# Kernel optimization log

Measured on AMD Instinct MI355X. Metric: run time of the kernel, lower is better.

Reference implementation:

```python
import jax, jax.numpy as jnp
import numpy as np

GROUPS = 8
EPS = 1e-5


def setup_inputs() -> dict:
    key = jax.random.key(0)
    ks = jax.random.split(key, 7)
    b, c, h, w = 32, 256, 32, 32
    x = jax.random.normal(ks[0], (b, c, h, w), dtype=jnp.float32)
    gn_weight = jax.random.normal(ks[1], (c,), dtype=jnp.float32) * 0.02 + 1.0
    gn_bias = jax.random.normal(ks[2], (c,), dtype=jnp.float32) * 0.02
    w_qkv = jax.random.normal(ks[3], (3 * c, c), dtype=jnp.float32) / np.sqrt(c)
    b_qkv = jax.random.normal(ks[4], (3 * c,), dtype=jnp.float32) * 0.01
    w_out = jax.random.normal(ks[5], (c, c), dtype=jnp.float32) / np.sqrt(c)
    b_out = jax.random.normal(ks[6], (c,), dtype=jnp.float32) * 0.01
    return {"x": x, "gn_weight": gn_weight, "gn_bias": gn_bias,
            "w_qkv": w_qkv, "b_qkv": b_qkv, "w_out": w_out, "b_out": b_out}


def group_norm(x, weight, bias):
    b, c, h, w = x.shape
    xg = x.reshape(b, GROUPS, c // GROUPS, h, w)
    mean = jnp.mean(xg, axis=(2, 3, 4), keepdims=True)
    var = jnp.var(xg, axis=(2, 3, 4), keepdims=True)
    xg = (xg - mean) * jax.lax.rsqrt(var + EPS)
    x = xg.reshape(b, c, h, w)
    return x * weight[None, :, None, None] + bias[None, :, None, None]


def reference(x, gn_weight, gn_bias, w_qkv, b_qkv, w_out, b_out):
    b, c, h, w = x.shape
    x_norm = group_norm(x, gn_weight, gn_bias)
    # 1x1 conv == channel matmul: (b, 3c, h, w)
    qkv = jnp.einsum('oc,bchw->bohw', w_qkv, x_norm) + b_qkv[None, :, None, None]
    q, k, v = jnp.split(qkv, 3, axis=1)
    hw = h * w
    q = q.reshape(b, c, hw)  # used transposed: (b, hw, c)
    k = k.reshape(b, c, hw)
    v = v.reshape(b, c, hw)
    scale = 1.0 / jnp.sqrt(jnp.float32(c))
    attn = jax.nn.softmax(jnp.einsum('bcs,bct->bst', q, k) * scale, axis=-1)  # (b, hw, hw)
    out = jnp.einsum('bst,bct->bcs', attn, v).reshape(b, c, h, w)
    out = jnp.einsum('oc,bchw->bohw', w_out, out) + b_out[None, :, None, None]
    return out + x
```

## Files before the change

### kernel.cpp

```cpp
#include <hip/hip_runtime.h>
#include <hip/hip_bf16.h>


typedef __bf16 bf16x8 __attribute__((ext_vector_type(8)));
typedef __bf16 bf16x4 __attribute__((ext_vector_type(4)));
typedef float f32x4 __attribute__((ext_vector_type(4)));
typedef float f32x16 __attribute__((ext_vector_type(16)));

#define MFMA16(a, b, c) __builtin_amdgcn_mfma_f32_16x16x32_bf16(a, b, c, 0, 0, 0)
#define MFMA32(a, b, c) __builtin_amdgcn_mfma_f32_32x32x16_bf16(a, b, c, 0, 0, 0)

#define GLD16(gsrc_, ldst_)                                                                  \
    __builtin_amdgcn_global_load_lds((const __attribute__((address_space(1))) void*)(gsrc_), \
                                     (__attribute__((address_space(3))) void*)(ldst_), 16, 0, 0)

__global__ __launch_bounds__(256) void gn_stats(const float* __restrict__ x,
                                                float* __restrict__ stats,
                                                const float* __restrict__ wqkv,
                                                const float* __restrict__ wout,
                                                __bf16* __restrict__ wbf) {
    const int bid = blockIdx.x, t = threadIdx.x;
    if (bid < 128) {
        int idx = (bid * 256 + t) * 8;
        const float* src = (idx < 196608) ? (wqkv + idx) : (wout + (idx - 196608));
        float4 v0 = *(const float4*)src;
        float4 v1 = *(const float4*)(src + 4);
        bf16x8 o;
        o[0] = (__bf16)v0.x; o[1] = (__bf16)v0.y; o[2] = (__bf16)v0.z; o[3] = (__bf16)v0.w;
        o[4] = (__bf16)v1.x; o[5] = (__bf16)v1.y; o[6] = (__bf16)v1.z; o[7] = (__bf16)v1.w;
        *(bf16x8*)&wbf[idx] = o;
    }
    const int bg = bid >> 3, part = bid & 7;
    const float* xp = x + (size_t)bg * 32768 + part * 4096;
    float s = 0.f, s2 = 0.f;
    #pragma unroll
    for (int i = 0; i < 4; i++) {
        float4 v = *(const float4*)(xp + (i * 256 + t) * 4);
        s  += v.x + v.y + v.z + v.w;
        s2 += v.x*v.x + v.y*v.y + v.z*v.z + v.w*v.w;
    }
    #pragma unroll
    for (int o = 32; o > 0; o >>= 1) { s += __shfl_down(s, o, 64); s2 += __shfl_down(s2, o, 64); }
    __shared__ float red[8];
    const int wv = t >> 6;
    if ((t & 63) == 0) { red[wv * 2] = s; red[wv * 2 + 1] = s2; }
    __syncthreads();
    if (t == 0) {
        float ts  = red[0] + red[2] + red[4] + red[6];
        float ts2 = red[1] + red[3] + red[5] + red[7];
        stats[bg * 16 + part * 2]     = ts;
        stats[bg * 16 + part * 2 + 1] = ts2;
    }
}

__global__ __launch_bounds__(512) void gn_apply(const float* __restrict__ x,
                                                const float* __restrict__ stats,
                                                const float* __restrict__ gw,
                                                const float* __restrict__ gb,
                                                __bf16* __restrict__ xnT) {
    const int bid = blockIdx.x;
    const int bg = bid >> 3, part = bid & 7;
    const int b = bg >> 3, g = bg & 7;
    const int t = threadIdx.x;
    float ts = 0.f, ts2 = 0.f;
    #pragma unroll
    for (int p = 0; p < 8; p++) { ts += stats[bg * 16 + p * 2]; ts2 += stats[bg * 16 + p * 2 + 1]; }
    const float mean = ts / 32768.f;
    const float inv = rsqrtf(ts2 / 32768.f - mean * mean + 1e-5f);
    __shared__ __bf16 Lds[128][48];
    const int c = t >> 4, ss = (t & 15) * 8;
    const float ga = gw[g * 32 + c], be = gb[g * 32 + c];
    const float* xp = x + (((size_t)b * 256 + g * 32 + c) * 1024) + part * 128 + ss;
    float4 v0 = *(const float4*)xp;
    float4 v1 = *(const float4*)(xp + 4);
    float vv[8] = {v0.x, v0.y, v0.z, v0.w, v1.x, v1.y, v1.z, v1.w};
    #pragma unroll
    for (int i = 0; i < 8; i++) Lds[ss + i][c] = (__bf16)((vv[i] - mean) * inv * ga + be);
    __syncthreads();
    const int row = t >> 2, cb = (t & 3) * 8;
    bf16x8 ov = *(const bf16x8*)&Lds[row][cb];
    *(bf16x8*)&xnT[((size_t)b * 1024 + part * 128 + row) * 256 + g * 32 + cb] = ov;
}

#define GEMM64G_BODY(ArowBase_, BrowBase_)                                              \
    f32x4 acc[4][4] = {};                                                               \
    for (int kk = 0; kk < 256; kk += 64) {                                              \
        _Pragma("unroll")                                                               \
        for (int i = 0; i < 4; i++) {                                                   \
            const int ch = wave * 4 + i;                                                \
            const int r = ch * 8 + (lane >> 3);                                         \
            const int sw = ((lane & 7) ^ (r & 7)) * 8;                                  \
            GLD16((ArowBase_) + (size_t)r * 256 + kk + sw, (char*)&As[0][0] + ch * 1024); \
            GLD16((BrowBase_) + (size_t)r * 256 + kk + sw, (char*)&Bs[0][0] + ch * 1024); \
        }                                                                               \
        __syncthreads();                                                                \
        _Pragma("unroll")                                                               \
        for (int kh = 0; kh < 2; kh++) {                                                \
            bf16x8 af[4], bfv[4];                                                       \
            _Pragma("unroll")                                                           \
            for (int im = 0; im < 4; im++) {                                            \
                const int row = wm + im * 16 + l16;                                     \
                af[im] = *(const bf16x8*)&As[row][(((kh * 4 + quad) ^ (row & 7)) * 8)]; \
            }                                                                           \
            _Pragma("unroll")                                                           \
            for (int in = 0; in < 4; in++) {                                            \
                const int row = wn + in * 16 + l16;                                     \
                bfv[in] = *(const bf16x8*)&Bs[row][(((kh * 4 + quad) ^ (row & 7)) * 8)]; \
            }                                                                           \
            _Pragma("unroll")                                                           \
            for (int im = 0; im < 4; im++)                                              \
                _Pragma("unroll")                                                       \
                for (int in = 0; in < 4; in++)                                          \
                    acc[im][in] = MFMA16(af[im], bfv[in], acc[im][in]);                 \
        }                                                                               \
        __syncthreads();                                                                \
    }

__global__ __launch_bounds__(256) void qkv_gemm(const __bf16* __restrict__ wbf,
                                                const float* __restrict__ bias,
                                                const __bf16* __restrict__ xnT,
                                                __bf16* __restrict__ qtr,
                                                __bf16* __restrict__ ktr,
                                                __bf16* __restrict__ vbuf) {
    __shared__ union {
        struct { __bf16 A[128][64]; __bf16 B[128][64]; } g;
        __bf16 ct[128][136];
    } sm;
    const int lin = blockIdx.x + ((blockIdx.y + blockIdx.z * 6) << 3);
    const int xcd = lin & 7, idx = lin >> 3;
    const int gwk = xcd * 192 + idx;
    const int mt = gwk % 6, panel = gwk / 6;
    const int b = panel >> 3;
    const int n0 = (panel & 7) * 128, m0 = mt * 128;
    const int t = threadIdx.x;
    const int wave = t >> 6, lane = t & 63, quad = lane >> 4, l16 = lane & 15;
    const int wm = (wave & 1) * 64, wn = (wave >> 1) * 64;
    const __bf16* arow = wbf + (size_t)m0 * 256;
    const __bf16* brow = xnT + ((size_t)b * 1024 + n0) * 256;
    auto As = sm.g.A;
    auto Bs = sm.g.B;

    GEMM64G_BODY(arow, brow)

    if (m0 < 512) {
        #pragma unroll
        for (int im = 0; im < 4; im++) {
            #pragma unroll
            for (int in = 0; in < 4; in++) {
                int ob = m0 + wm + im * 16 + quad * 4;
                bf16x4 ov;
                #pragma unroll
                for (int r = 0; r < 4; r++) ov[r] = (__bf16)(acc[im][in][r] + bias[ob + r]);
                *(bf16x4*)&sm.ct[wn + in * 16 + l16][wm + im * 16 + quad * 4] = ov;
            }
        }
        __syncthreads();
        {
            const int rbase = t >> 2, cf = t & 3;
            #pragma unroll
            for (int rr = 0; rr < 2; rr++) {
                int row = rbase + rr * 64;
                int sg = n0 + row;
                __bf16* dst = (m0 < 256) ? &qtr[((size_t)b * 1024 + sg) * 256 + m0]
                                         : &ktr[((size_t)b * 1024 + sg) * 256 + (m0 - 256)];
                #pragma unroll
                for (int u = 0; u < 4; u++) {
                    int colb = cf * 8 + u * 32;
                    *(bf16x8*)&dst[colb] = *(const bf16x8*)&sm.ct[row][colb];
                }
            }
        }
    } else {
        #pragma unroll
        for (int im = 0; im < 4; im++) {
            #pragma unroll
            for (int in = 0; in < 4; in++) {
                int cl = wm + im * 16 + quad * 4;
                int tl = wn + in * 16 + l16;
                #pragma unroll
                for (int r = 0; r < 4; r++)
                    sm.ct[cl + r][tl] = (__bf16)(acc[im][in][r] + bias[m0 + cl + r]);
            }
        }
        __syncthreads();
        {
            const int row = t >> 1, tc = (t & 1) * 64;
            const int cglob = m0 - 512 + row;
            __bf16* dst = &vbuf[((size_t)b * 256 + cglob) * 1024 + n0 + tc];
            #pragma unroll
            for (int u = 0; u < 8; u++)
                *(bf16x8*)&dst[u * 8] = *(const bf16x8*)&sm.ct[row][tc + u * 8];
        }
    }
}

__global__ __launch_bounds__(512, 2) void attn_kernel(const __bf16* __restrict__ qtr,
                                                      const __bf16* __restrict__ ktr,
                                                      const __bf16* __restrict__ vbuf,
                                                      __bf16* __restrict__ aoT) {
    __shared__ __bf16 Kt[2][32][260];
    __shared__ __bf16 Vs[2][256][36];
    __shared__ bf16x8 Pl[4][2][2][64];
    __shared__ float Lred[4][2][32];
    const int b = blockIdx.x;
    const int tid = threadIdx.x;
    const int wave = tid >> 6, lane = tid & 63, half = lane >> 5, l31 = lane & 31;
    const int pair = wave & 3, th = wave >> 2;
    const int s0 = blockIdx.y * 128 + pair * 32;
    const float kscale = 0.09016844f;

    bf16x8 aq[16];
    #pragma unroll
    for (int ks = 0; ks < 16; ks++)
        aq[ks] = *(const bf16x8*)&qtr[((size_t)b * 1024 + s0 + l31) * 256 + ks * 16 + half * 8];

    const int k_row = tid >> 3;
    const int k_cb  = (tid & 7) * 8;
    const int v_c   = tid >> 1;
    const int v_th  = tid & 1;
    const size_t kbase = (size_t)b * 1024 * 256;
    const size_t vbase = (size_t)b * 256 * 1024;

    float l_acc = 0.f;
    f32x16 o_acc[4] = {};

    bf16x8 kpre[4], vpre[4];
    #pragma unroll
    for (int u = 0; u < 4; u++) {
        kpre[u] = *(const bf16x8*)&ktr[kbase + (size_t)k_row * 256 + k_cb + u * 64];
        vpre[u] = *(const bf16x8*)&vbuf[vbase + (size_t)v_c * 1024 + v_th * 32 + u * 8];
    }

    for (int it = 0; it < 16; it++) {
        #pragma unroll
        for (int u = 0; u < 4; u++)
            *(bf16x8*)&Kt[k_row >> 5][k_row & 31][k_cb + u * 64] = kpre[u];
        #pragma unroll
        for (int u = 0; u < 4; u++) {
            const bf16x4* hv = (const bf16x4*)&vpre[u];
            const int sbase = (u >> 1) * 16 + (u & 1) * 4;
            *(bf16x4*)&Vs[v_th][v_c][sbase]     = hv[0];
            *(bf16x4*)&Vs[v_th][v_c][sbase + 8] = hv[1];
        }
        __syncthreads();
        if (it < 15) {
            const int t1 = (it + 1) * 64;
            #pragma unroll
            for (int u = 0; u < 4; u++) {
                kpre[u] = *(const bf16x8*)&ktr[kbase + (size_t)(t1 + k_row) * 256 + k_cb + u * 64];
                vpre[u] = *(const bf16x8*)&vbuf[vbase + (size_t)v_c * 1024 + t1 + v_th * 32 + u * 8];
            }
        }

        f32x16 sc_a = {}, sc_b = {};
        __builtin_amdgcn_s_setprio(1);
        #pragma unroll
        for (int ks = 0; ks < 8; ks++) {
            bf16x8 bk0 = *(const bf16x8*)&Kt[th][l31][ks * 16 + half * 8];
            bf16x8 bk1 = *(const bf16x8*)&Kt[th][l31][(ks + 8) * 16 + half * 8];
            sc_a = MFMA32(bk0, aq[ks], sc_a);
            sc_b = MFMA32(bk1, aq[ks + 8], sc_b);
        }
        __builtin_amdgcn_s_setprio(0);

        bf16x8 pf0, pf1;
        #pragma unroll
        for (int r = 0; r < 8; r++) {
            float p = exp2f((sc_a[r] + sc_b[r]) * kscale);
            l_acc += p;
            pf0[r] = (__bf16)p;
        }
        #pragma unroll
        for (int r = 8; r < 16; r++) {
            float p = exp2f((sc_a[r] + sc_b[r]) * kscale);
            l_acc += p;
            pf1[r - 8] = (__bf16)p;
        }
        Pl[pair][th][0][lane] = pf0;
        Pl[pair][th][1][lane] = pf1;
        __syncthreads();
        bf16x8 pp0 = Pl[pair][1 - th][0][lane];
        bf16x8 pp1 = Pl[pair][1 - th][1][lane];

        bf16x8 ap[4];
        if (th == 0) { ap[0] = pf0; ap[1] = pf1; ap[2] = pp0; ap[3] = pp1; }
        else         { ap[0] = pp0; ap[1] = pp1; ap[2] = pf0; ap[3] = pf1; }

        __builtin_amdgcn_s_setprio(1);
        #pragma unroll
        for (int n = 0; n < 4; n++) {
            int c = th * 128 + n * 32 + l31;
            #pragma unroll
            for (int kc = 0; kc < 4; kc++) {
                bf16x8 bv = *(const bf16x8*)&Vs[kc >> 1][c][(kc & 1) * 16 + half * 8];
                o_acc[n] = MFMA32(ap[kc], bv, o_acc[n]);
            }
        }
        __builtin_amdgcn_s_setprio(0);
        __syncthreads();
    }

    l_acc += __shfl_xor(l_acc, 32, 64);
    if (lane < 32) Lred[pair][th][l31] = l_acc;
    __syncthreads();
    #pragma unroll
    for (int r = 0; r < 16; r++) {
        int row = (r & 3) + 8 * (r >> 2) + 4 * half;
        float rinv = 1.0f / (Lred[pair][0][row] + Lred[pair][1][row]);
        #pragma unroll
        for (int n = 0; n < 4; n++) {
            int c = th * 128 + n * 32 + l31;
            aoT[((size_t)b * 1024 + s0 + row) * 256 + c] = (__bf16)(o_acc[n][r] * rinv);
        }
    }
}

__global__ __launch_bounds__(256) void proj_gemm(const __bf16* __restrict__ wbf_out,
                                                 const float* __restrict__ bias,
                                                 const __bf16* __restrict__ aoT,
                                                 const float* __restrict__ resid,
                                                 float* __restrict__ Out) {
    __shared__ union {
        struct { __bf16 A[128][64]; __bf16 B[128][64]; } g;
        float cf[64][132];
    } sm;
    const int lin = blockIdx.x + ((blockIdx.y + blockIdx.z * 2) << 3);
    const int xcd = lin & 7, idx = lin >> 3;
    const int gwk = xcd * 64 + idx;
    const int mt = gwk & 1, panel = gwk >> 1;
    const int b = panel >> 3;
    const int n0 = (panel & 7) * 128, m0 = mt * 128;
    const int t = threadIdx.x;
    const int wave = t >> 6, lane = t & 63, quad = lane >> 4, l16 = lane & 15;
    const int wm = (wave & 1) * 64, wn = (wave >> 1) * 64;
    const __bf16* arow = wbf_out + (size_t)m0 * 256;
    const __bf16* brow = aoT + ((size_t)b * 1024 + n0) * 256;
    auto As = sm.g.A;
    auto Bs = sm.g.B;

    GEMM64G_BODY(arow, brow)

    for (int h = 0; h < 2; h++) {
        if ((wave & 1) == h) {
            #pragma unroll
            for (int im = 0; im < 4; im++)
                #pragma unroll
                for (int in = 0; in < 4; in++)
                    #pragma unroll
                    for (int r = 0; r < 4; r++)
                        sm.cf[im * 16 + quad * 4 + r][wn + in * 16 + l16] = acc[im][in][r];
        }
        __syncthreads();
        {
            const int rloc = t >> 2, cq = (t & 3) * 4;
            const int o = m0 + h * 64 + rloc;
            const float bo = bias[o];
            const float* rrow = &resid[((size_t)b * 256 + o) * 1024 + n0];
            float* orow = &Out[((size_t)b * 256 + o) * 1024 + n0];
            #pragma unroll
            for (int u = 0; u < 8; u++) {
                int col = cq + u * 16;
                f32x4 cv = *(const f32x4*)&sm.cf[rloc][col];
                float4 rv = *(const float4*)&rrow[col];
                float4 ov;
                ov.x = cv[0] + bo + rv.x;
                ov.y = cv[1] + bo + rv.y;
                ov.z = cv[2] + bo + rv.z;
                ov.w = cv[3] + bo + rv.w;
                *(float4*)&orow[col] = ov;
            }
        }
        __syncthreads();
    }
}

extern "C" void kernel_launch(void* const* d_in, const int* in_sizes, int n_in,
                              void* d_out, int out_size, void* d_ws, size_t ws_size,
                              hipStream_t stream) {
    const float* x    = (const float*)d_in[0];
    const float* gw   = (const float*)d_in[1];
    const float* gb   = (const float*)d_in[2];
    const float* wqkv = (const float*)d_in[3];
    const float* bqkv = (const float*)d_in[4];
    const float* wout = (const float*)d_in[5];
    const float* bout = (const float*)d_in[6];
    float* out = (float*)d_out;

    const size_t T16 = (size_t)32 * 1024 * 256;
    __bf16* xnT  = (__bf16*)d_ws;
    __bf16* qtr  = xnT + T16;
    __bf16* ktr  = qtr + T16;
    __bf16* vbuf = ktr + T16;
    __bf16* aoT  = vbuf + T16;
    __bf16* wbf  = aoT + T16;
    float* gstats = (float*)(wbf + 262144);

    gn_stats<<<dim3(2048), 256, 0, stream>>>(x, gstats, wqkv, wout, wbf);
    gn_apply<<<dim3(2048), 512, 0, stream>>>(x, gstats, gw, gb, xnT);
    qkv_gemm<<<dim3(8, 6, 32), 256, 0, stream>>>(wbf, bqkv, xnT, qtr, ktr, vbuf);
    attn_kernel<<<dim3(32, 8), 512, 0, stream>>>(qtr, ktr, vbuf, aoT);
    proj_gemm<<<dim3(8, 2, 32), 256, 0, stream>>>(wbf + 196608, bout, aoT, x, out);
}
```

Measured before the change: 186.4 us.

## Double-buffer LDS tiles in QKV and projection GEMMs; vectorize gn_apply LDS writes

Result: no change. 185.2 us (-0.6%).

```diff
diff --git a/kernel.cpp b/kernel.cpp
--- a/kernel.cpp
+++ b/kernel.cpp
@@ -67,45 +67,67 @@
     for (int p = 0; p < 8; p++) { ts += stats[bg * 16 + p * 2]; ts2 += stats[bg * 16 + p * 2 + 1]; }
     const float mean = ts / 32768.f;
     const float inv = rsqrtf(ts2 / 32768.f - mean * mean + 1e-5f);
-    __shared__ __bf16 Lds[128][48];
+    __shared__ __bf16 Lds[32][136];
     const int c = t >> 4, ss = (t & 15) * 8;
     const float ga = gw[g * 32 + c], be = gb[g * 32 + c];
     const float* xp = x + (((size_t)b * 256 + g * 32 + c) * 1024) + part * 128 + ss;
     float4 v0 = *(const float4*)xp;
     float4 v1 = *(const float4*)(xp + 4);
     float vv[8] = {v0.x, v0.y, v0.z, v0.w, v1.x, v1.y, v1.z, v1.w};
-    #pragma unroll
-    for (int i = 0; i < 8; i++) Lds[ss + i][c] = (__bf16)((vv[i] - mean) * inv * ga + be);
+    bf16x8 wv;
+    #pragma unroll
+    for (int i = 0; i < 8; i++) wv[i] = (__bf16)((vv[i] - mean) * inv * ga + be);
+    *(bf16x8*)&Lds[c][ss] = wv;
     __syncthreads();
     const int row = t >> 2, cb = (t & 3) * 8;
-    bf16x8 ov = *(const bf16x8*)&Lds[row][cb];
+    bf16x8 ov;
+    #pragma unroll
+    for (int j = 0; j < 8; j++) ov[j] = Lds[cb + j][row];
     *(bf16x8*)&xnT[((size_t)b * 1024 + part * 128 + row) * 256 + g * 32 + cb] = ov;
 }
 
-#define GEMM64G_BODY(ArowBase_, BrowBase_)                                              \
+#define GEMM64P_BODY(ArowBase_, BrowBase_)                                              \
     f32x4 acc[4][4] = {};                                                               \
-    for (int kk = 0; kk < 256; kk += 64) {                                              \
+    {                                                                                   \
         _Pragma("unroll")                                                               \
         for (int i = 0; i < 4; i++) {                                                   \
             const int ch = wave * 4 + i;                                                \
             const int r = ch * 8 + (lane >> 3);                                         \
             const int sw = ((lane & 7) ^ (r & 7)) * 8;                                  \
-            GLD16((ArowBase_) + (size_t)r * 256 + kk + sw, (char*)&As[0][0] + ch * 1024); \
-            GLD16((BrowBase_) + (size_t)r * 256 + kk + sw, (char*)&Bs[0][0] + ch * 1024); \
+            GLD16((ArowBase_) + (size_t)r * 256 + sw, (char*)&As[0][0][0] + ch * 1024); \
+            GLD16((BrowBase_) + (size_t)r * 256 + sw, (char*)&Bs[0][0][0] + ch * 1024); \
         }                                                                               \
-        __syncthreads();                                                                \
+    }                                                                                   \
+    _Pragma("unroll")                                                                   \
+    for (int kk = 0; kk < 4; kk++) {                                                    \
+        if (kk < 3) {                                                                   \
+            _Pragma("unroll")                                                           \
+            for (int i = 0; i < 4; i++) {                                               \
+                const int ch = wave * 4 + i;                                            \
+                const int r = ch * 8 + (lane >> 3);                                     \
+                const int sw = ((lane & 7) ^ (r & 7)) * 8;                              \
+                GLD16((ArowBase_) + (size_t)r * 256 + (kk + 1) * 64 + sw,               \
+                      (char*)&As[(kk + 1) & 1][0][0] + ch * 1024);                      \
+                GLD16((BrowBase_) + (size_t)r * 256 + (kk + 1) * 64 + sw,               \
+                      (char*)&Bs[(kk + 1) & 1][0][0] + ch * 1024);                      \
+            }                                                                           \
+            asm volatile("s_waitcnt vmcnt(8)" ::: "memory");                            \
+        } else {                                                                        \
+            asm volatile("s_waitcnt vmcnt(0)" ::: "memory");                            \
+        }                                                                               \
+        asm volatile("s_barrier" ::: "memory");                                         \
         _Pragma("unroll")                                                               \
         for (int kh = 0; kh < 2; kh++) {                                                \
             bf16x8 af[4], bfv[4];                                                       \
             _Pragma("unroll")                                                           \
             for (int im = 0; im < 4; im++) {                                            \
                 const int row = wm + im * 16 + l16;                                     \
-                af[im] = *(const bf16x8*)&As[row][(((kh * 4 + quad) ^ (row & 7)) * 8)]; \
+                af[im] = *(const bf16x8*)&As[kk & 1][row][(((kh * 4 + quad) ^ (row & 7)) * 8)]; \
             }                                                                           \
             _Pragma("unroll")                                                           \
             for (int in = 0; in < 4; in++) {                                            \
                 const int row = wn + in * 16 + l16;                                     \
-                bfv[in] = *(const bf16x8*)&Bs[row][(((kh * 4 + quad) ^ (row & 7)) * 8)]; \
+                bfv[in] = *(const bf16x8*)&Bs[kk & 1][row][(((kh * 4 + quad) ^ (row & 7)) * 8)]; \
             }                                                                           \
             _Pragma("unroll")                                                           \
             for (int im = 0; im < 4; im++)                                              \
@@ -113,7 +135,8 @@
                 for (int in = 0; in < 4; in++)                                          \
                     acc[im][in] = MFMA16(af[im], bfv[in], acc[im][in]);                 \
         }                                                                               \
-        __syncthreads();                                                                \
+        asm volatile("s_waitcnt lgkmcnt(0)" ::: "memory");                              \
+        asm volatile("s_barrier" ::: "memory");                                        \
     }
 
 __global__ __launch_bounds__(256) void qkv_gemm(const __bf16* __restrict__ wbf,
@@ -123,7 +146,7 @@
                                                 __bf16* __restrict__ ktr,
                                                 __bf16* __restrict__ vbuf) {
     __shared__ union {
-        struct { __bf16 A[128][64]; __bf16 B[128][64]; } g;
+        struct { __bf16 A[2][128][64]; __bf16 B[2][128][64]; } g;
         __bf16 ct[128][136];
     } sm;
     const int lin = blockIdx.x + ((blockIdx.y + blockIdx.z * 6) << 3);
@@ -140,7 +163,7 @@
     auto As = sm.g.A;
     auto Bs = sm.g.B;
 
-    GEMM64G_BODY(arow, brow)
+    GEMM64P_BODY(arow, brow)
 
     if (m0 < 512) {
         #pragma unroll
@@ -321,7 +344,7 @@
                                                  const float* __restrict__ resid,
                                                  float* __restrict__ Out) {
     __shared__ union {
-        struct { __bf16 A[128][64]; __bf16 B[128][64]; } g;
+        struct { __bf16 A[2][128][64]; __bf16 B[2][128][64]; } g;
         float cf[64][132];
     } sm;
     const int lin = blockIdx.x + ((blockIdx.y + blockIdx.z * 2) << 3);
@@ -338,7 +361,7 @@
     auto As = sm.g.A;
     auto Bs = sm.g.B;
 
-    GEMM64G_BODY(arow, brow)
+    GEMM64P_BODY(arow, brow)
 
     for (int h = 0; h < 2; h++) {
         if ((wave & 1) == h) {
```
